# Kernel tuning notes

Measured on AMD Instinct MI355X. Metric: run time of the kernel, lower is better.

Reference implementation:

```python
import jax, jax.numpy as jnp
import numpy as np

N = 50000      # nodes
E = 800000     # edges (before self-loops)
IN_DIM = 128
HID = 96
PROJ = 64
BN_EPS = 1e-5
L2_EPS = 1e-12


def setup_inputs() -> dict:
    key = jax.random.key(0)
    ks = jax.random.split(key, 8)

    def glorot(k, shape):
        fan_in, fan_out = shape
        s = np.sqrt(6.0 / (fan_in + fan_out)).astype(np.float32)
        return jax.random.uniform(k, shape, jnp.float32, -s, s)

    x = jax.random.normal(ks[0], (N, IN_DIM), jnp.float32)
    edge_index = jax.random.randint(ks[1], (2, E), 0, N, dtype=jnp.int64)

    return {
        "x": x,
        "edge_index": edge_index,
        # GCN layer 1
        "W1": glorot(ks[2], (IN_DIM, HID)), "b1": jnp.zeros(HID, jnp.float32),
        "g1": jnp.ones(HID, jnp.float32), "be1": jnp.zeros(HID, jnp.float32),
        # GCN layer 2
        "W2": glorot(ks[3], (HID, HID)), "b2": jnp.zeros(HID, jnp.float32),
        "g2": jnp.ones(HID, jnp.float32), "be2": jnp.zeros(HID, jnp.float32),
        # projector: Linear -> BN -> ReLU -> Linear
        "Wp1": glorot(ks[4], (HID, HID)), "bp1": jnp.zeros(HID, jnp.float32),
        "gp": jnp.ones(HID, jnp.float32), "bep": jnp.zeros(HID, jnp.float32),
        "Wp2": glorot(ks[5], (HID, PROJ)), "bp2": jnp.zeros(PROJ, jnp.float32),
    }


def _batchnorm(h, gamma, beta):
    # training-mode BatchNorm1d: batch stats, biased variance
    m = h.mean(axis=0)
    v = h.var(axis=0)
    return gamma * (h - m) * jax.lax.rsqrt(v + BN_EPS) + beta


def _gcn_conv(x, W, b, src, dst, deg_inv_sqrt):
    # PyG GCNConv: x @ W, symmetric-normalized scatter-add (self-loops included
    # in src/dst), then bias.
    xw = x @ W                                              # [N, out]
    norm = deg_inv_sqrt[src] * deg_inv_sqrt[dst]            # [E+N]
    msg = xw[src] * norm[:, None]                           # [E+N, out]
    out = jax.ops.segment_sum(msg, dst, num_segments=x.shape[0])
    return out + b


def reference(x, edge_index, W1, b1, g1, be1, W2, b2, g2, be2,
              Wp1, bp1, gp, bep, Wp2, bp2):
    n = x.shape[0]
    loops = jnp.arange(n, dtype=edge_index.dtype)
    src = jnp.concatenate([edge_index[0], loops])
    dst = jnp.concatenate([edge_index[1], loops])
    deg = jax.ops.segment_sum(jnp.ones(src.shape[0], x.dtype), dst,
                              num_segments=n)               # includes self-loops
    deg_inv_sqrt = jax.lax.rsqrt(deg)                       # deg >= 1 always

    h = jax.nn.relu(_batchnorm(_gcn_conv(x, W1, b1, src, dst, deg_inv_sqrt), g1, be1))
    h = jax.nn.relu(_batchnorm(_gcn_conv(h, W2, b2, src, dst, deg_inv_sqrt), g2, be2))

    z = jax.nn.relu(_batchnorm(h @ Wp1 + bp1, gp, bep))
    z = z @ Wp2 + bp2
    # F.normalize(p=2, dim=-1, eps=1e-12)
    nrm = jnp.linalg.norm(z, axis=-1, keepdims=True)
    return z / jnp.maximum(nrm, L2_EPS)
```

## Files before the change

kernel.cpp:

```cpp
#include <hip/hip_runtime.h>
#include <hip/hip_fp16.h>

constexpr int BLK = 256;

static inline int cdiv(long long a, int b) { return (int)((a + b - 1) / b); }

using v8h = __attribute__((ext_vector_type(8))) _Float16;
using v4f = __attribute__((ext_vector_type(4))) float;



__global__ __launch_bounds__(256) void scan1_dis(const int* __restrict__ cnt,
                                                 int* __restrict__ rowptr,
                                                 int* __restrict__ bsum,
                                                 float* __restrict__ dis, int N) {
    __shared__ int ts[256];
    int tid = threadIdx.x;
    int base = blockIdx.x * 1024 + tid * 4;
    int v[4], s = 0;
#pragma unroll
    for (int i = 0; i < 4; ++i) {
        v[i] = (base + i < N) ? cnt[base + i] : 0;
        s += v[i];
        if (base + i < N) dis[base + i] = rsqrtf((float)v[i] + 1.0f);
    }
    ts[tid] = s;
    __syncthreads();
    for (int off = 1; off < 256; off <<= 1) {
        int t = 0;
        if (tid >= off) t = ts[tid - off];
        __syncthreads();
        if (tid >= off) ts[tid] += t;
        __syncthreads();
    }
    int run = ts[tid] - s;
#pragma unroll
    for (int i = 0; i < 4; ++i) {
        if (base + i < N) rowptr[base + i] = run;
        run += v[i];
    }
    if (tid == 255) bsum[blockIdx.x] = ts[255];
}

__global__ __launch_bounds__(256) void scan23(int* __restrict__ rowptr,
                                              const int* __restrict__ bsum,
                                              int nb, int N, int E) {
    __shared__ int sboff[64];
    const int tid = threadIdx.x;
    if (tid < 64) {
        int orig = (tid < nb) ? bsum[tid] : 0;
        int v = orig;
#pragma unroll
        for (int off = 1; off < 64; off <<= 1) {
            int t = __shfl_up(v, off, 64);
            if (tid >= off) v += t;
        }
        sboff[tid] = v - orig;
    }
    __syncthreads();
    int i = blockIdx.x * 256 + tid;
    if (i < N) rowptr[i] += sboff[i >> 10];
    if (i == 0) rowptr[N] = E;
}

__global__ void csr_fill(const int* __restrict__ src, const int* __restrict__ dst,
                         const unsigned short* __restrict__ eoff,
                         const int* __restrict__ rowptr,
                         unsigned short* __restrict__ csrc, int E) {
    for (int i = blockIdx.x * blockDim.x + threadIdx.x; i < E; i += gridDim.x * blockDim.x) {
        csrc[rowptr[dst[i]] + (int)eoff[i]] = (unsigned short)src[i];
    }
}


template <int K, bool ACT, bool BIAS, bool STATS, typename TIN>
__device__ __forceinline__ void gemm96_body(int bid,
                                            const TIN* __restrict__ in,
                                            const float* __restrict__ W,
                                            const float* __restrict__ bias,
                                            const float* __restrict__ bnsums,
                                            const float* __restrict__ gamma,
                                            const float* __restrict__ beta,
                                            const float* __restrict__ dsc,
                                            _Float16* __restrict__ hout,
                                            float* __restrict__ osums, int N) {
    constexpr int NK = K / 32;
    constexpr int LDK = K + 8;
    __shared__ __align__(16) _Float16 Wt[96 * LDK];
    __shared__ __align__(16) float ssl[ACT ? 192 : 1];
    __shared__ float sb[STATS ? 192 : 1];
    const int tid = threadIdx.x;
    for (int idx = tid; idx < K * 96; idx += 256) {
        int k = idx / 96, n = idx - k * 96;
        Wt[n * LDK + k] = (_Float16)W[idx];
    }
    if (ACT && tid < 96) {
        float inv_n = 1.0f / (float)N;
        float mean = bnsums[tid] * inv_n;
        float var = bnsums[96 + tid] * inv_n - mean * mean;
        float sc = gamma[tid] * rsqrtf(var + 1e-5f);
        ssl[tid] = sc;
        ssl[96 + tid] = beta[tid] - mean * sc;
    }
    if (STATS && tid < 192) sb[tid] = 0.0f;
    __syncthreads();

    const int wave = tid >> 6, lane = tid & 63;
    const int quad = lane >> 4, lm = lane & 15;
    const int rbase = bid * 64 + wave * 16;
    int arow = rbase + lm;
    arow = arow < N ? arow : N - 1;

    v8h afr[NK];
#pragma unroll
    for (int kc = 0; kc < NK; ++kc) {
        const int kk = kc * 32 + quad * 8;
        if constexpr (sizeof(TIN) == 4) {
            const float* p = (const float*)&in[(long long)arow * K + kk];
            float4 p0 = *(const float4*)p;
            float4 p1 = *(const float4*)(p + 4);
            if (ACT) {
                float4 sc0 = *(const float4*)&ssl[kk];
                float4 sc1 = *(const float4*)&ssl[kk + 4];
                float4 sh0 = *(const float4*)&ssl[96 + kk];
                float4 sh1 = *(const float4*)&ssl[96 + kk + 4];
                p0.x = fmaxf(fmaf(p0.x, sc0.x, sh0.x), 0.0f);
                p0.y = fmaxf(fmaf(p0.y, sc0.y, sh0.y), 0.0f);
                p0.z = fmaxf(fmaf(p0.z, sc0.z, sh0.z), 0.0f);
                p0.w = fmaxf(fmaf(p0.w, sc0.w, sh0.w), 0.0f);
                p1.x = fmaxf(fmaf(p1.x, sc1.x, sh1.x), 0.0f);
                p1.y = fmaxf(fmaf(p1.y, sc1.y, sh1.y), 0.0f);
                p1.z = fmaxf(fmaf(p1.z, sc1.z, sh1.z), 0.0f);
                p1.w = fmaxf(fmaf(p1.w, sc1.w, sh1.w), 0.0f);
            }
            v8h a;
            a[0] = (_Float16)p0.x; a[1] = (_Float16)p0.y;
            a[2] = (_Float16)p0.z; a[3] = (_Float16)p0.w;
            a[4] = (_Float16)p1.x; a[5] = (_Float16)p1.y;
            a[6] = (_Float16)p1.z; a[7] = (_Float16)p1.w;
            afr[kc] = a;
        } else {
            v8h hv = *(const v8h*)&in[((long long)kc * N + arow) * 32 + quad * 8];
            if (ACT) {
#pragma unroll
                for (int j = 0; j < 8; ++j) {
                    float f = (float)hv[j];
                    f = fmaxf(fmaf(f, ssl[kk + j], ssl[96 + kk + j]), 0.0f);
                    hv[j] = (_Float16)f;
                }
            }
            afr[kc] = hv;
        }
    }

    v4f acc[6];
#pragma unroll
    for (int t = 0; t < 6; ++t) {
        v4f c = {0.0f, 0.0f, 0.0f, 0.0f};
#pragma unroll
        for (int kc = 0; kc < NK; ++kc) {
            v8h b = *(const v8h*)&Wt[(t * 16 + lm) * LDK + kc * 32 + quad * 8];
            c = __builtin_amdgcn_mfma_f32_16x16x32_f16(afr[kc], b, c, 0, 0, 0);
        }
        acc[t] = c;
    }

    float dr[4];
#pragma unroll
    for (int r = 0; r < 4; ++r) {
        int gr = rbase + quad * 4 + r;
        dr[r] = dsc ? dsc[gr < N ? gr : N - 1] : 1.0f;
    }

    float ls[6], lq[6];
#pragma unroll
    for (int t = 0; t < 6; ++t) { ls[t] = 0.0f; lq[t] = 0.0f; }
#pragma unroll
    for (int t = 0; t < 6; ++t) {
        float bv = BIAS ? bias[t * 16 + lm] : 0.0f;
        const long long pbase = (long long)(t >> 1) * N;
        const int cw = (t & 1) * 16 + lm;
#pragma unroll
        for (int r = 0; r < 4; ++r) {
            int gr = rbase + quad * 4 + r;
            if (gr < N) {
                float o = acc[t][r] + bv;
                hout[(pbase + gr) * 32 + cw] = (_Float16)(o * dr[r]);
                if (STATS) { ls[t] += o; lq[t] += o * o; }
            }
        }
    }
    if (STATS) {
#pragma unroll
        for (int t = 0; t < 6; ++t) {
            ls[t] += __shfl_xor(ls[t], 16);
            ls[t] += __shfl_xor(ls[t], 32);
            lq[t] += __shfl_xor(lq[t], 16);
            lq[t] += __shfl_xor(lq[t], 32);
        }
        if (quad == 0) {
#pragma unroll
            for (int t = 0; t < 6; ++t) {
                atomicAdd(&sb[t * 16 + lm], ls[t]);
                atomicAdd(&sb[96 + t * 16 + lm], lq[t]);
            }
        }
        __syncthreads();
        if (tid < 192) atomicAdd(&osums[tid], sb[tid]);
    }
}

template <int K, bool ACT, bool BIAS, bool STATS, typename TIN>
__global__ __launch_bounds__(256) void gemm96m(const TIN* __restrict__ in,
                                               const float* __restrict__ W,
                                               const float* __restrict__ bias,
                                               const float* __restrict__ bnsums,
                                               const float* __restrict__ gamma,
                                               const float* __restrict__ beta,
                                               const float* __restrict__ dsc,
                                               _Float16* __restrict__ hout,
                                               float* __restrict__ osums, int N) {
    gemm96_body<K, ACT, BIAS, STATS, TIN>(blockIdx.x, in, W, bias, bnsums,
                                          gamma, beta, dsc, hout, osums, N);
}

__global__ __launch_bounds__(256) void gemm1_count(const float* __restrict__ x,
                                                   const float* __restrict__ W1,
                                                   _Float16* __restrict__ hout,
                                                   const int* __restrict__ dst,
                                                   int* __restrict__ cnt,
                                                   unsigned short* __restrict__ eoff,
                                                   int gG, int N, int E) {
    if ((int)blockIdx.x < gG) {
        gemm96_body<128, false, false, false, float>(
            blockIdx.x, x, W1, nullptr, nullptr, nullptr, nullptr, nullptr,
            hout, nullptr, N);
    } else {
        int g = (blockIdx.x - gG) * 256 + threadIdx.x;
        int stride = (gridDim.x - gG) * 256;
        for (int i = g; i < E; i += stride)
            eoff[i] = (unsigned short)atomicAdd(&cnt[dst[i]], 1);
    }
}


__global__ __launch_bounds__(256) void gemm_finalm(const _Float16* __restrict__ in,
                                                   const float* __restrict__ W,
                                                   const float* __restrict__ bias,
                                                   const float* __restrict__ bnsums,
                                                   const float* __restrict__ gamma,
                                                   const float* __restrict__ beta,
                                                   float* __restrict__ out, int N) {
    constexpr int K = 96, NK = 3, LDK = K + 8;
    __shared__ __align__(16) _Float16 Wt[64 * LDK];
    __shared__ __align__(16) float ssl[192];
    const int tid = threadIdx.x;
    for (int idx = tid; idx < K * 64; idx += 256) {
        int k = idx / 64, n = idx - k * 64;
        Wt[n * LDK + k] = (_Float16)W[idx];
    }
    if (tid < 96) {
        float inv_n = 1.0f / (float)N;
        float mean = bnsums[tid] * inv_n;
        float var = bnsums[96 + tid] * inv_n - mean * mean;
        float sc = gamma[tid] * rsqrtf(var + 1e-5f);
        ssl[tid] = sc;
        ssl[96 + tid] = beta[tid] - mean * sc;
    }
    __syncthreads();

    const int wave = tid >> 6, lane = tid & 63;
    const int quad = lane >> 4, lm = lane & 15;
    const int rbase = blockIdx.x * 64 + wave * 16;
    int arow = rbase + lm;
    arow = arow < N ? arow : N - 1;

    v8h afr[NK];
#pragma unroll
    for (int kc = 0; kc < NK; ++kc) {
        const int kk = kc * 32 + quad * 8;
        v8h hv = *(const v8h*)&in[((long long)kc * N + arow) * 32 + quad * 8];
#pragma unroll
        for (int j = 0; j < 8; ++j) {
            float f = (float)hv[j];
            f = fmaxf(fmaf(f, ssl[kk + j], ssl[96 + kk + j]), 0.0f);
            hv[j] = (_Float16)f;
        }
        afr[kc] = hv;
    }

    v4f acc[4];
#pragma unroll
    for (int t = 0; t < 4; ++t) {
        v4f c = {0.0f, 0.0f, 0.0f, 0.0f};
#pragma unroll
        for (int kc = 0; kc < NK; ++kc) {
            v8h b = *(const v8h*)&Wt[(t * 16 + lm) * LDK + kc * 32 + quad * 8];
            c = __builtin_amdgcn_mfma_f32_16x16x32_f16(afr[kc], b, c, 0, 0, 0);
        }
        float bv = bias[t * 16 + lm];
        c[0] += bv; c[1] += bv; c[2] += bv; c[3] += bv;
        acc[t] = c;
    }

    float sq[4];
#pragma unroll
    for (int r = 0; r < 4; ++r) {
        float s = acc[0][r] * acc[0][r] + acc[1][r] * acc[1][r] +
                  acc[2][r] * acc[2][r] + acc[3][r] * acc[3][r];
#pragma unroll
        for (int m = 1; m < 16; m <<= 1) s += __shfl_xor(s, m, 64);
        sq[r] = 1.0f / fmaxf(sqrtf(s), 1e-12f);
    }
#pragma unroll
    for (int r = 0; r < 4; ++r) {
        int gr = rbase + quad * 4 + r;
        if (gr < N) {
#pragma unroll
            for (int t = 0; t < 4; ++t)
                out[(long long)gr * 64 + t * 16 + lm] = acc[t][r] * sq[r];
        }
    }
}


template <bool PRESC>
__global__ __launch_bounds__(256) void agg32p(const __half* __restrict__ hxw,
                                              const int* __restrict__ rowptr,
                                              const unsigned short* __restrict__ csrc,
                                              const float* __restrict__ dis,
                                              const float* __restrict__ bias,
                                              _Float16* __restrict__ outh,
                                              int nchp, int N) {
    int nwg = gridDim.x;
    int wid = (blockIdx.x & 7) * (nwg >> 3) + (blockIdx.x >> 3);
    int plane = wid / nchp, chunk = wid - plane * nchp;
    int colth = threadIdx.x & 3;
    int n = chunk * 64 + (threadIdx.x >> 2);
    if (n >= N) return;
    const __half* hp = hxw + (long long)plane * N * 32 + colth * 8;
    float dn = dis[n];
    float acc[8];
    {
        float sw = PRESC ? 1.0f : dn;
        float4 g = *(const float4*)&hp[n * 32];
        const __half2* hs = (const __half2*)&g;
#pragma unroll
        for (int k = 0; k < 4; ++k) {
            float2 f = __half22float2(hs[k]);
            acc[2 * k + 0] = f.x * sw;
            acc[2 * k + 1] = f.y * sw;
        }
    }
    int e = rowptr[n], e1 = rowptr[n + 1];
    for (; e + 7 < e1; e += 8) {
        int s[8];
        float4 g[8];
        float w[8];
#pragma unroll
        for (int j = 0; j < 8; ++j) s[j] = csrc[e + j];
        if (!PRESC) {
#pragma unroll
            for (int j = 0; j < 8; ++j) w[j] = dis[s[j]];
        }
#pragma unroll
        for (int j = 0; j < 8; ++j) g[j] = *(const float4*)&hp[s[j] * 32];
#pragma unroll
        for (int j = 0; j < 8; ++j) {
            const __half2* h = (const __half2*)&g[j];
#pragma unroll
            for (int k = 0; k < 4; ++k) {
                float2 f = __half22float2(h[k]);
                if (PRESC) { acc[2 * k] += f.x; acc[2 * k + 1] += f.y; }
                else {
                    acc[2 * k]     = fmaf(f.x, w[j], acc[2 * k]);
                    acc[2 * k + 1] = fmaf(f.y, w[j], acc[2 * k + 1]);
                }
            }
        }
    }
    for (; e + 3 < e1; e += 4) {
        int s[4];
        float4 g[4];
        float w[4];
#pragma unroll
        for (int j = 0; j < 4; ++j) s[j] = csrc[e + j];
        if (!PRESC) {
#pragma unroll
            for (int j = 0; j < 4; ++j) w[j] = dis[s[j]];
        }
#pragma unroll
        for (int j = 0; j < 4; ++j) g[j] = *(const float4*)&hp[s[j] * 32];
#pragma unroll
        for (int j = 0; j < 4; ++j) {
            const __half2* h = (const __half2*)&g[j];
#pragma unroll
            for (int k = 0; k < 4; ++k) {
                float2 f = __half22float2(h[k]);
                if (PRESC) { acc[2 * k] += f.x; acc[2 * k + 1] += f.y; }
                else {
                    acc[2 * k]     = fmaf(f.x, w[j], acc[2 * k]);
                    acc[2 * k + 1] = fmaf(f.y, w[j], acc[2 * k + 1]);
                }
            }
        }
    }
    for (; e < e1; ++e) {
        int s0 = csrc[e];
        float w0 = PRESC ? 1.0f : dis[s0];
        float4 g0 = *(const float4*)&hp[s0 * 32];
        const __half2* h = (const __half2*)&g0;
#pragma unroll
        for (int k = 0; k < 4; ++k) {
            float2 f = __half22float2(h[k]);
            acc[2 * k]     = fmaf(f.x, w0, acc[2 * k]);
            acc[2 * k + 1] = fmaf(f.y, w0, acc[2 * k + 1]);
        }
    }
    const int ch = plane * 32 + colth * 8;
    v8h o;
#pragma unroll
    for (int j = 0; j < 8; ++j)
        o[j] = (_Float16)fmaf(acc[j], dn, bias[ch + j]);
    *(v8h*)&outh[((long long)plane * N + n) * 32 + colth * 8] = o;
}


__global__ __launch_bounds__(256) void bn_statsp(const __half* __restrict__ h,
                                                 float* __restrict__ sums,
                                                 int nchp, int N) {
    __shared__ float sb[64];
    const int tid = threadIdx.x;
    if (tid < 64) sb[tid] = 0.0f;
    __syncthreads();
    int plane = blockIdx.x / nchp, chunk = blockIdx.x - plane * nchp;
    int colth = tid & 3;
    int n = chunk * 64 + (tid >> 2);
    float s[8] = {0, 0, 0, 0, 0, 0, 0, 0};
    float q[8] = {0, 0, 0, 0, 0, 0, 0, 0};
    if (n < N) {
        float4 raw = *(const float4*)&h[((long long)plane * N + n) * 32 + colth * 8];
        const __half2* hp = (const __half2*)&raw;
#pragma unroll
        for (int k = 0; k < 4; ++k) {
            float2 f = __half22float2(hp[k]);
            s[2 * k + 0] = f.x;  s[2 * k + 1] = f.y;
            q[2 * k + 0] = f.x * f.x;  q[2 * k + 1] = f.y * f.y;
        }
    }
#pragma unroll
    for (int j = 0; j < 8; ++j) {
#pragma unroll
        for (int m = 4; m < 64; m <<= 1) {
            s[j] += __shfl_xor(s[j], m, 64);
            q[j] += __shfl_xor(q[j], m, 64);
        }
    }
    if ((tid & 63) < 4) {
#pragma unroll
        for (int j = 0; j < 8; ++j) {
            atomicAdd(&sb[colth * 8 + j], s[j]);
            atomicAdd(&sb[32 + colth * 8 + j], q[j]);
        }
    }
    __syncthreads();
    if (tid < 64)
        atomicAdd(&sums[(tid >> 5) * 96 + plane * 32 + (tid & 31)], sb[tid]);
}


extern "C" void kernel_launch(void* const* d_in, const int* in_sizes, int n_in,
                              void* d_out, int out_size, void* d_ws, size_t ws_size,
                              hipStream_t stream) {
    const float* x   = (const float*)d_in[0];
    const int*   ei  = (const int*)d_in[1];
    const float* W1  = (const float*)d_in[2];
    const float* b1  = (const float*)d_in[3];
    const float* g1  = (const float*)d_in[4];
    const float* be1 = (const float*)d_in[5];
    const float* W2  = (const float*)d_in[6];
    const float* b2  = (const float*)d_in[7];
    const float* g2  = (const float*)d_in[8];
    const float* be2 = (const float*)d_in[9];
    const float* Wp1 = (const float*)d_in[10];
    const float* bp1 = (const float*)d_in[11];
    const float* gp  = (const float*)d_in[12];
    const float* bep = (const float*)d_in[13];
    const float* Wp2 = (const float*)d_in[14];
    const float* bp2 = (const float*)d_in[15];

    const int N = in_sizes[0] / 128;
    const int E = in_sizes[1] / 2;
    const int* src = ei;
    const int* dst = ei + E;

    char* w = (char*)d_ws;
    auto alloc = [&](size_t bytes) { char* p = w; w += (bytes + 15) & ~size_t(15); return p; };
    int*            cnt    = (int*)alloc((size_t)N * 4);
    float*          sums   = (float*)alloc(576 * 4);
    int*            rowptr = (int*)alloc((size_t)(N + 1) * 4);
    int*            bsum   = (int*)alloc(64 * 4);
    float*          dis    = (float*)alloc((size_t)N * 4);
    unsigned short* eoff   = (unsigned short*)alloc((size_t)E * 2);
    unsigned short* csrc   = (unsigned short*)alloc((size_t)E * 2);
    _Float16*       buf2h  = (_Float16*)alloc((size_t)N * 96 * 2);
    _Float16*       hbuf   = (_Float16*)alloc((size_t)N * 96 * 2);
    float* sums1 = sums, *sums2 = sums + 192, *sums3 = sums + 384;

    float* out = (float*)d_out;

    const int gE   = cdiv(E, BLK);
    const int gG   = cdiv(N, 64);
    const int gC   = 1024;
    const int nb   = cdiv(N, 1024);
    const int nchp = (cdiv(N, 64) + 7) & ~7;
    const int gAgg = 3 * nchp;

    size_t zlen = (size_t)((char*)sums - (char*)cnt) + 576 * 4;
    hipMemsetAsync(cnt, 0, zlen, stream);

    gemm1_count<<<gG + gC, 256, 0, stream>>>(x, W1, hbuf, dst, cnt, eoff, gG, N, E);
    scan1_dis<<<nb, 256, 0, stream>>>(cnt, rowptr, bsum, dis, N);
    scan23<<<cdiv(N, 256), 256, 0, stream>>>(rowptr, bsum, nb, N, E);
    csr_fill<<<gE, BLK, 0, stream>>>(src, dst, eoff, rowptr, csrc, E);

    agg32p<false><<<gAgg, 256, 0, stream>>>((const __half*)hbuf, rowptr, csrc, dis,
                                            b1, buf2h, nchp, N);
    bn_statsp<<<gAgg, 256, 0, stream>>>((const __half*)buf2h, sums1, nchp, N);

    gemm96m<96, true, false, false, _Float16><<<gG, 256, 0, stream>>>(
        buf2h, W2, nullptr, sums1, g1, be1, dis, hbuf, nullptr, N);
    agg32p<true><<<gAgg, 256, 0, stream>>>((const __half*)hbuf, rowptr, csrc, dis,
                                           b2, buf2h, nchp, N);
    bn_statsp<<<gAgg, 256, 0, stream>>>((const __half*)buf2h, sums2, nchp, N);

    gemm96m<96, true, true, true, _Float16><<<gG, 256, 0, stream>>>(
        buf2h, Wp1, bp1, sums2, g2, be2, nullptr, hbuf, sums3, N);

    gemm_finalm<<<gG, 256, 0, stream>>>(hbuf, Wp2, bp2, sums3, gp, bep, out, N);
}
```

Baseline: 319.0 us.

## Store aggregation outputs row-major and use grid-stride BN stats kernel

The aggregation kernels now write their fp16 outputs in row-major [N,96] layout instead of three 32-column planes. The GEMM loaders and the final GEMM read that row-major layout, and the last projector GEMM writes row-major output. The plane-based BN stats kernel is replaced by a grid-stride kernel with a fixed grid of 510 blocks. Each thread accumulates in registers before doing shared-memory atomics, which cuts per-element shuffle reductions but adds more LDS atomic contention per thread.

```diff
diff --git a/kernel.cpp b/kernel.cpp
--- a/kernel.cpp
+++ b/kernel.cpp
@@ -73,7 +73,7 @@
 }
 
 
-template <int K, bool ACT, bool BIAS, bool STATS, typename TIN>
+template <int K, bool ACT, bool BIAS, bool STATS, bool OUTSP, typename TIN>
 __device__ __forceinline__ void gemm96_body(int bid,
                                             const TIN* __restrict__ in,
                                             const float* __restrict__ W,
@@ -140,7 +140,7 @@
             a[6] = (_Float16)p1.z; a[7] = (_Float16)p1.w;
             afr[kc] = a;
         } else {
-            v8h hv = *(const v8h*)&in[((long long)kc * N + arow) * 32 + quad * 8];
+            v8h hv = *(const v8h*)&in[(long long)arow * 96 + kk];
             if (ACT) {
 #pragma unroll
                 for (int j = 0; j < 8; ++j) {
@@ -178,14 +178,17 @@
 #pragma unroll
     for (int t = 0; t < 6; ++t) {
         float bv = BIAS ? bias[t * 16 + lm] : 0.0f;
-        const long long pbase = (long long)(t >> 1) * N;
-        const int cw = (t & 1) * 16 + lm;
 #pragma unroll
         for (int r = 0; r < 4; ++r) {
             int gr = rbase + quad * 4 + r;
             if (gr < N) {
                 float o = acc[t][r] + bv;
-                hout[(pbase + gr) * 32 + cw] = (_Float16)(o * dr[r]);
+                if (OUTSP) {
+                    hout[(((long long)(t >> 1) * N + gr) * 32) + (t & 1) * 16 + lm] =
+                        (_Float16)(o * dr[r]);
+                } else {
+                    hout[(long long)gr * 96 + t * 16 + lm] = (_Float16)(o * dr[r]);
+                }
                 if (STATS) { ls[t] += o; lq[t] += o * o; }
             }
         }
@@ -210,7 +213,7 @@
     }
 }
 
-template <int K, bool ACT, bool BIAS, bool STATS, typename TIN>
+template <int K, bool ACT, bool BIAS, bool STATS, bool OUTSP, typename TIN>
 __global__ __launch_bounds__(256) void gemm96m(const TIN* __restrict__ in,
                                                const float* __restrict__ W,
                                                const float* __restrict__ bias,
@@ -220,8 +223,8 @@
                                                const float* __restrict__ dsc,
                                                _Float16* __restrict__ hout,
                                                float* __restrict__ osums, int N) {
-    gemm96_body<K, ACT, BIAS, STATS, TIN>(blockIdx.x, in, W, bias, bnsums,
-                                          gamma, beta, dsc, hout, osums, N);
+    gemm96_body<K, ACT, BIAS, STATS, OUTSP, TIN>(blockIdx.x, in, W, bias, bnsums,
+                                                 gamma, beta, dsc, hout, osums, N);
 }
 
 __global__ __launch_bounds__(256) void gemm1_count(const float* __restrict__ x,
@@ -232,7 +235,7 @@
                                                    unsigned short* __restrict__ eoff,
                                                    int gG, int N, int E) {
     if ((int)blockIdx.x < gG) {
-        gemm96_body<128, false, false, false, float>(
+        gemm96_body<128, false, false, false, true, float>(
             blockIdx.x, x, W1, nullptr, nullptr, nullptr, nullptr, nullptr,
             hout, nullptr, N);
     } else {
@@ -279,7 +282,7 @@
 #pragma unroll
     for (int kc = 0; kc < NK; ++kc) {
         const int kk = kc * 32 + quad * 8;
-        v8h hv = *(const v8h*)&in[((long long)kc * N + arow) * 32 + quad * 8];
+        v8h hv = *(const v8h*)&in[(long long)arow * 96 + kk];
 #pragma unroll
         for (int j = 0; j < 8; ++j) {
             float f = (float)hv[j];
@@ -422,50 +425,41 @@
 #pragma unroll
     for (int j = 0; j < 8; ++j)
         o[j] = (_Float16)fmaf(acc[j], dn, bias[ch + j]);
-    *(v8h*)&outh[((long long)plane * N + n) * 32 + colth * 8] = o;
-}
-
-
-__global__ __launch_bounds__(256) void bn_statsp(const __half* __restrict__ h,
-                                                 float* __restrict__ sums,
-                                                 int nchp, int N) {
-    __shared__ float sb[64];
+    *(v8h*)&outh[(long long)n * 96 + ch] = o;
+}
+
+
+__global__ __launch_bounds__(256) void bn_stats96h(const __half* __restrict__ h,
+                                                   float* __restrict__ sums, int N) {
+    __shared__ float sb[192];
     const int tid = threadIdx.x;
-    if (tid < 64) sb[tid] = 0.0f;
+    if (tid < 192) sb[tid] = 0.0f;
     __syncthreads();
-    int plane = blockIdx.x / nchp, chunk = blockIdx.x - plane * nchp;
-    int colth = tid & 3;
-    int n = chunk * 64 + (tid >> 2);
+    int g = blockIdx.x * 256 + tid;
+    int total = N * 12, stride = gridDim.x * 256;
+    int c8 = g % 12;
     float s[8] = {0, 0, 0, 0, 0, 0, 0, 0};
     float q[8] = {0, 0, 0, 0, 0, 0, 0, 0};
-    if (n < N) {
-        float4 raw = *(const float4*)&h[((long long)plane * N + n) * 32 + colth * 8];
+    for (int i = g; i < total; i += stride) {
+        int n = i / 12;
+        float4 raw = *(const float4*)&h[n * 96 + 8 * c8];
         const __half2* hp = (const __half2*)&raw;
 #pragma unroll
         for (int k = 0; k < 4; ++k) {
             float2 f = __half22float2(hp[k]);
-            s[2 * k + 0] = f.x;  s[2 * k + 1] = f.y;
-            q[2 * k + 0] = f.x * f.x;  q[2 * k + 1] = f.y * f.y;
+            s[2 * k + 0] += f.x;
+            s[2 * k + 1] += f.y;
+            q[2 * k + 0] += f.x * f.x;
+            q[2 * k + 1] += f.y * f.y;
         }
     }
 #pragma unroll
     for (int j = 0; j < 8; ++j) {
-#pragma unroll
-        for (int m = 4; m < 64; m <<= 1) {
-            s[j] += __shfl_xor(s[j], m, 64);
-            q[j] += __shfl_xor(q[j], m, 64);
-        }
-    }
-    if ((tid & 63) < 4) {
-#pragma unroll
-        for (int j = 0; j < 8; ++j) {
-            atomicAdd(&sb[colth * 8 + j], s[j]);
-            atomicAdd(&sb[32 + colth * 8 + j], q[j]);
-        }
+        atomicAdd(&sb[8 * c8 + j], s[j]);
+        atomicAdd(&sb[96 + 8 * c8 + j], q[j]);
     }
     __syncthreads();
-    if (tid < 64)
-        atomicAdd(&sums[(tid >> 5) * 96 + plane * 32 + (tid & 31)], sb[tid]);
+    if (tid < 192) atomicAdd(&sums[tid], sb[tid]);
 }
 
 
@@ -526,15 +520,15 @@
 
     agg32p<false><<<gAgg, 256, 0, stream>>>((const __half*)hbuf, rowptr, csrc, dis,
                                             b1, buf2h, nchp, N);
-    bn_statsp<<<gAgg, 256, 0, stream>>>((const __half*)buf2h, sums1, nchp, N);
-
-    gemm96m<96, true, false, false, _Float16><<<gG, 256, 0, stream>>>(
+    bn_stats96h<<<510, 256, 0, stream>>>((const __half*)buf2h, sums1, N);
+
+    gemm96m<96, true, false, false, true, _Float16><<<gG, 256, 0, stream>>>(
         buf2h, W2, nullptr, sums1, g1, be1, dis, hbuf, nullptr, N);
     agg32p<true><<<gAgg, 256, 0, stream>>>((const __half*)hbuf, rowptr, csrc, dis,
                                            b2, buf2h, nchp, N);
-    bn_statsp<<<gAgg, 256, 0, stream>>>((const __half*)buf2h, sums2, nchp, N);
-
-    gemm96m<96, true, true, true, _Float16><<<gG, 256, 0, stream>>>(
+    bn_stats96h<<<510, 256, 0, stream>>>((const __half*)buf2h, sums2, N);
+
+    gemm96m<96, true, true, true, false, _Float16><<<gG, 256, 0, stream>>>(
         buf2h, Wp1, bp1, sums2, g2, be2, nullptr, hbuf, sums3, N);
 
     gemm_finalm<<<gG, 256, 0, stream>>>(hbuf, Wp2, bp2, sums3, gp, bep, out, N);
```

New measurement: 311.4 us. 2.4% less time.
